# Optimization experiments

Hardware: AMD Instinct MI355X
Metric: run time of the kernel (lower is better)

Reference implementation:

```python
import jax, jax.numpy as jnp
import numpy as np

N_NODES = 200_000
N_EDGES = 3_200_000
N_GRAPHS = 512
D_IN, D_HID, D_OUT = 2, 64, 3


def setup_inputs() -> dict:
    key = jax.random.key(0)
    k = jax.random.split(key, 7)
    x = jax.random.normal(k[0], (N_NODES, D_IN), dtype=jnp.float32)
    edge_index = jax.random.randint(k[1], (2, N_EDGES), 0, N_NODES)
    batch = jnp.sort(jax.random.randint(k[2], (N_NODES,), 0, N_GRAPHS))
    W1 = jax.random.normal(k[3], (D_IN, D_HID), dtype=jnp.float32) * (1.0 / np.sqrt(D_IN))
    b1 = jnp.zeros((D_HID,), dtype=jnp.float32)
    W2 = jax.random.normal(k[4], (D_HID, D_OUT), dtype=jnp.float32) * (1.0 / np.sqrt(D_HID))
    b2 = jnp.zeros((D_OUT,), dtype=jnp.float32)
    return {"x": x, "edge_index": edge_index, "batch": batch,
            "W1": W1, "b1": b1, "W2": W2, "b2": b2}


def reference(x, edge_index, batch, W1, b1, W2, b2):
    n = x.shape[0]
    loop = jnp.arange(n, dtype=edge_index.dtype)
    src = jnp.concatenate([edge_index[0], loop])  # [E+N] with self-loops
    dst = jnp.concatenate([edge_index[1], loop])
    # symmetric normalization D^{-1/2} (A+I) D^{-1/2} (PyG GCNConv default)
    deg = jax.ops.segment_sum(jnp.ones_like(dst, dtype=x.dtype), dst, num_segments=n)
    dinv = jax.lax.rsqrt(jnp.maximum(deg, 1.0))
    norm = (dinv[src] * dinv[dst])[:, None]  # [E+N, 1]

    def gcn_conv(h, W, b):
        h = h @ W                                    # [N, d_out]
        msg = h[src] * norm                          # gather + scale
        agg = jax.ops.segment_sum(msg, dst, num_segments=n)  # scatter-add
        return agg + b

    h = jax.nn.relu(gcn_conv(x, W1, b1))
    h = gcn_conv(h, W2, b2)                          # [N, 3]

    # global mean pool over graphs in the batch
    cnt = jax.ops.segment_sum(jnp.ones((n,), h.dtype), batch, num_segments=N_GRAPHS)
    pooled = jax.ops.segment_sum(h, batch, num_segments=N_GRAPHS)
    pooled = pooled / jnp.maximum(cnt, 1.0)[:, None]  # [G, 3]
    return jax.nn.log_softmax(pooled, axis=1)
```

## Files before the change

kernel.cpp:

```cpp
#include <hip/hip_runtime.h>

#define NBLK 1024
#define PTH  512
#define SH   9
#define BUCK 512
#define NBUK_MAX 512
#define SCB  512
#define PREP_CAP 10240


__global__ void __launch_bounds__(PTH) k_pcount(const int* __restrict__ dst,
                                                int* __restrict__ hist2d,
                                                int E, int nbuk, int chunk) {
    __shared__ int h[NBUK_MAX];
    for (int t = threadIdx.x; t < nbuk; t += PTH) h[t] = 0;
    __syncthreads();
    int beg = blockIdx.x * chunk, end = min(beg + chunk, E);
    for (int i = beg + threadIdx.x; i < end; i += PTH)
        atomicAdd(&h[dst[i] >> SH], 1);
    __syncthreads();
    for (int t = threadIdx.x; t < nbuk; t += PTH)
        hist2d[t * NBLK + blockIdx.x] = h[t];
}

__global__ void __launch_bounds__(SCB) k_scanA(const int* __restrict__ in,
                                               int* __restrict__ outp,
                                               int* __restrict__ bsum, int M) {
    __shared__ int s[SCB];
    int t = threadIdx.x, i = blockIdx.x * SCB + t;
    int h = (i < M) ? in[i] : 0;
    s[t] = h; __syncthreads();
    for (int off = 1; off < SCB; off <<= 1) {
        int v = (t >= off) ? s[t - off] : 0;
        __syncthreads();
        s[t] += v;
        __syncthreads();
    }
    if (i < M) outp[i] = s[t] - h;
    if (t == SCB - 1) bsum[blockIdx.x] = s[SCB - 1];
}

__global__ void k_scanB(const int* __restrict__ bsum, int* __restrict__ bsum_ex, int NB) {
    __shared__ int s[1024];
    int t = threadIdx.x;
    int v = (t < NB) ? bsum[t] : 0;
    s[t] = v; __syncthreads();
    for (int off = 1; off < 1024; off <<= 1) {
        int u = (t >= off) ? s[t - off] : 0;
        __syncthreads();
        s[t] += u;
        __syncthreads();
    }
    if (t < NB) bsum_ex[t] = s[t] - v;
}

__device__ __forceinline__ int scan_off(const int* rs2, const int* bse, int j) {
    return rs2[j] + bse[j >> 9];
}

__global__ void __launch_bounds__(PTH) k_pfill(const int* __restrict__ src,
                                               const int* __restrict__ dst,
                                               const int* __restrict__ rs2,
                                               const int* __restrict__ bse,
                                               int* __restrict__ part,
                                               int E, int nbuk, int chunk) {
    __shared__ int cur[NBUK_MAX];
    for (int t = threadIdx.x; t < nbuk; t += PTH)
        cur[t] = scan_off(rs2, bse, t * NBLK + blockIdx.x);
    __syncthreads();
    int beg = blockIdx.x * chunk, end = min(beg + chunk, E);
    for (int i = beg + threadIdx.x; i < end; i += PTH) {
        int d = dst[i];
        int pos = atomicAdd(&cur[d >> SH], 1);
        part[pos] = (src[i] << SH) | (d & (BUCK - 1));
    }
}

__global__ void __launch_bounds__(512) k_prep(
        const int* __restrict__ part, const int* __restrict__ rs2,
        const int* __restrict__ bse, const float* __restrict__ x,
        int* __restrict__ part2, int* __restrict__ rowstart,
        float* __restrict__ dinv, float2* __restrict__ xw,
        int n, int nbuk, int E) {
    __shared__ int hist[BUCK];
    __shared__ int s[BUCK];
    __shared__ int cur[BUCK];
    __shared__ int outbuf[PREP_CAP];
    int t = threadIdx.x, b = blockIdx.x;
    hist[t] = 0;
    __syncthreads();
    int beg = scan_off(rs2, bse, b * NBLK);
    int end = (b + 1 < nbuk) ? scan_off(rs2, bse, (b + 1) * NBLK) : E;
    for (int i = beg + t; i < end; i += 512)
        atomicAdd(&hist[part[i] & (BUCK - 1)], 1);
    __syncthreads();
    s[t] = hist[t];
    __syncthreads();
    for (int d = 1; d < 512; d <<= 1) {
        int v = (t >= d) ? s[t - d] : 0;
        __syncthreads();
        s[t] += v;
        __syncthreads();
    }
    int excl = s[t] - hist[t];
    cur[t] = beg + excl;
    int node = (b << SH) + t;
    rowstart[node] = beg + excl;
    if (node < n) {
        float di = rsqrtf((float)hist[t] + 1.0f);
        dinv[node] = di;
        float2 xs = *reinterpret_cast<const float2*>(&x[2 * node]);
        xw[node] = make_float2(di * xs.x, di * xs.y);
    }
    __syncthreads();
    int cnt = end - beg;
    bool staged = (cnt <= PREP_CAP);
    if (staged) {
        for (int i = beg + t; i < end; i += 512) {
            int e = part[i];
            int p = atomicAdd(&cur[e & (BUCK - 1)], 1);
            outbuf[p - beg] = e >> SH;
        }
        __syncthreads();
        for (int i = t; i < cnt; i += 512)
            part2[beg + i] = outbuf[i];
    } else {
        for (int i = beg + t; i < end; i += 512) {
            int e = part[i];
            int p = atomicAdd(&cur[e & (BUCK - 1)], 1);
            part2[p] = e >> SH;
        }
    }
}

__global__ void __launch_bounds__(256) k_bz(
        const int* __restrict__ part2, const int* __restrict__ rowstart,
        const float* __restrict__ dinv, const float2* __restrict__ xw,
        const float* __restrict__ W1, const float* __restrict__ b1,
        const float* __restrict__ W2, float4* __restrict__ zw, int n) {
    __shared__ float sW1[128], sb1[64], sW2[192];
    for (int t = threadIdx.x; t < 128; t += 256) sW1[t] = W1[t];
    for (int t = threadIdx.x; t < 64;  t += 256) sb1[t] = b1[t];
    for (int t = threadIdx.x; t < 192; t += 256) sW2[t] = W2[t];
    __syncthreads();
    int tid = blockIdx.x * 256 + threadIdx.x;
    int i = tid >> 2, lane = tid & 3;
    if (i >= n) return;
    int beg = rowstart[i], end = rowstart[i + 1];
    float a0 = 0.f, a1 = 0.f;
    int e = beg + lane;
    for (; e + 4 < end; e += 8) {
        int s0 = part2[e];
        int s1 = part2[e + 4];
        float2 v0 = xw[s0];
        float2 v1 = xw[s1];
        a0 += v0.x + v1.x;
        a1 += v0.y + v1.y;
    }
    if (e < end) {
        float2 v = xw[part2[e]];
        a0 += v.x; a1 += v.y;
    }
    if (lane == 0) {
        float2 self = xw[i];
        a0 += self.x; a1 += self.y;
    }
    a0 += __shfl_xor(a0, 1); a0 += __shfl_xor(a0, 2);
    a1 += __shfl_xor(a1, 1); a1 += __shfl_xor(a1, 2);
    float di = dinv[i];
    a0 *= di; a1 *= di;
    float z0 = 0.f, z1 = 0.f, z2 = 0.f;
    int j0 = lane << 4;
#pragma unroll
    for (int jj = 0; jj < 16; ++jj) {
        int j = j0 + jj;
        float h = fmaf(a0, sW1[j], fmaf(a1, sW1[64 + j], sb1[j]));
        h = fmaxf(h, 0.f);
        z0 = fmaf(h, sW2[3 * j],     z0);
        z1 = fmaf(h, sW2[3 * j + 1], z1);
        z2 = fmaf(h, sW2[3 * j + 2], z2);
    }
    z0 += __shfl_xor(z0, 1); z0 += __shfl_xor(z0, 2);
    z1 += __shfl_xor(z1, 1); z1 += __shfl_xor(z1, 2);
    z2 += __shfl_xor(z2, 1); z2 += __shfl_xor(z2, 2);
    if (lane == 0)
        zw[i] = make_float4(di * z0, di * z1, di * z2, 0.f);
}

__global__ void __launch_bounds__(256) k_bout(
        const int* __restrict__ part2, const int* __restrict__ rowstart,
        const float* __restrict__ dinv, const float4* __restrict__ zw,
        const float* __restrict__ b2, const int* __restrict__ batch,
        float* __restrict__ pooled, float* __restrict__ cnt, int n) {
    int tid = blockIdx.x * 256 + threadIdx.x;
    int i = tid >> 2, lane = tid & 3;
    float o0 = 0.f, o1 = 0.f, o2 = 0.f, vc = 0.f;
    int g = -1;
    if (i < n) {
        int beg = rowstart[i], end = rowstart[i + 1];
        float a0 = 0.f, a1 = 0.f, a2 = 0.f;
        int e = beg + lane;
        for (; e + 4 < end; e += 8) {
            int s0 = part2[e];
            int s1 = part2[e + 4];
            float4 v0 = zw[s0];
            float4 v1 = zw[s1];
            a0 += v0.x + v1.x;
            a1 += v0.y + v1.y;
            a2 += v0.z + v1.z;
        }
        if (e < end) {
            float4 v = zw[part2[e]];
            a0 += v.x; a1 += v.y; a2 += v.z;
        }
        if (lane == 0) {
            float4 self = zw[i];
            a0 += self.x; a1 += self.y; a2 += self.z;
        }
        a0 += __shfl_xor(a0, 1); a0 += __shfl_xor(a0, 2);
        a1 += __shfl_xor(a1, 1); a1 += __shfl_xor(a1, 2);
        a2 += __shfl_xor(a2, 1); a2 += __shfl_xor(a2, 2);
        if (lane == 0) {
            float di = dinv[i];
            o0 = fmaf(di, a0, b2[0]);
            o1 = fmaf(di, a1, b2[1]);
            o2 = fmaf(di, a2, b2[2]);
            vc = 1.f;
        }
        g = batch[i];
    }
    int g0 = __shfl(g, 0);
    bool uni = __all(g == g0);
    if (uni) {
        for (int off = 32; off; off >>= 1) {
            o0 += __shfl_down(o0, off);
            o1 += __shfl_down(o1, off);
            o2 += __shfl_down(o2, off);
            vc += __shfl_down(vc, off);
        }
        if ((threadIdx.x & 63) == 0 && g0 >= 0) {
            atomicAdd(&pooled[3 * g0],     o0);
            atomicAdd(&pooled[3 * g0 + 1], o1);
            atomicAdd(&pooled[3 * g0 + 2], o2);
            atomicAdd(&cnt[g0], vc);
        }
    } else if (g >= 0 && lane == 0) {
        atomicAdd(&pooled[3 * g],     o0);
        atomicAdd(&pooled[3 * g + 1], o1);
        atomicAdd(&pooled[3 * g + 2], o2);
        atomicAdd(&cnt[g], 1.f);
    }
}

__global__ void k_out(const float* __restrict__ pooled, const float* __restrict__ cnt,
                      float* __restrict__ out, int G) {
    int g = blockIdx.x * blockDim.x + threadIdx.x;
    if (g >= G) return;
    float c = fmaxf(cnt[g], 1.0f);
    float p0 = pooled[3 * g] / c, p1 = pooled[3 * g + 1] / c, p2 = pooled[3 * g + 2] / c;
    float m = fmaxf(p0, fmaxf(p1, p2));
    float s = expf(p0 - m) + expf(p1 - m) + expf(p2 - m);
    float l = logf(s);
    out[3 * g]     = p0 - m - l;
    out[3 * g + 1] = p1 - m - l;
    out[3 * g + 2] = p2 - m - l;
}


__global__ void kB_deg(const int* __restrict__ dst, float* __restrict__ deg, int E) {
    int i = blockIdx.x * blockDim.x + threadIdx.x;
    if (i < E) atomicAdd(&deg[dst[i]], 1.0f);
}

__global__ void kB_dinv(float* __restrict__ deg, int n) {
    int i = blockIdx.x * blockDim.x + threadIdx.x;
    if (i < n) deg[i] = rsqrtf(deg[i] + 1.0f);
}

__global__ void kB_agg1(const int* __restrict__ src, const int* __restrict__ dst,
                        const float* __restrict__ dinv, const float* __restrict__ x,
                        float* __restrict__ agg1, int E) {
    int i = blockIdx.x * blockDim.x + threadIdx.x;
    if (i >= E) return;
    int s = src[i], d = dst[i];
    float w = dinv[s] * dinv[d];
    float2 xs = *reinterpret_cast<const float2*>(&x[2 * s]);
    atomicAdd(&agg1[2 * d],     w * xs.x);
    atomicAdd(&agg1[2 * d + 1], w * xs.y);
}

__global__ void kB_z(const float* __restrict__ agg1, const float* __restrict__ x,
                     const float* __restrict__ dinv,
                     const float* __restrict__ W1, const float* __restrict__ b1,
                     const float* __restrict__ W2, float* __restrict__ z, int n) {
    __shared__ float sW1[128], sb1[64], sW2[192];
    for (int t = threadIdx.x; t < 128; t += blockDim.x) sW1[t] = W1[t];
    for (int t = threadIdx.x; t < 64;  t += blockDim.x) sb1[t] = b1[t];
    for (int t = threadIdx.x; t < 192; t += blockDim.x) sW2[t] = W2[t];
    __syncthreads();
    int i = blockIdx.x * blockDim.x + threadIdx.x;
    if (i >= n) return;
    float di = dinv[i], w = di * di;
    float2 xs = *reinterpret_cast<const float2*>(&x[2 * i]);
    float a0 = agg1[2 * i]     + w * xs.x;
    float a1 = agg1[2 * i + 1] + w * xs.y;
    float z0 = 0.f, z1 = 0.f, z2 = 0.f;
#pragma unroll
    for (int j = 0; j < 64; ++j) {
        float h = fmaf(a0, sW1[j], fmaf(a1, sW1[64 + j], sb1[j]));
        h = fmaxf(h, 0.f);
        z0 = fmaf(h, sW2[3 * j],     z0);
        z1 = fmaf(h, sW2[3 * j + 1], z1);
        z2 = fmaf(h, sW2[3 * j + 2], z2);
    }
    z[3 * i] = z0; z[3 * i + 1] = z1; z[3 * i + 2] = z2;
}

__global__ void kB_agg2(const int* __restrict__ src, const int* __restrict__ dst,
                        const float* __restrict__ dinv, const float* __restrict__ z,
                        float* __restrict__ agg2, int E) {
    int i = blockIdx.x * blockDim.x + threadIdx.x;
    if (i >= E) return;
    int s = src[i], d = dst[i];
    float w = dinv[s] * dinv[d];
    atomicAdd(&agg2[3 * d],     w * z[3 * s]);
    atomicAdd(&agg2[3 * d + 1], w * z[3 * s + 1]);
    atomicAdd(&agg2[3 * d + 2], w * z[3 * s + 2]);
}

__global__ void kB_pool(const float* __restrict__ agg2, const float* __restrict__ z,
                        const float* __restrict__ dinv, const float* __restrict__ b2,
                        const int* __restrict__ batch,
                        float* __restrict__ pooled, float* __restrict__ cnt, int n) {
    int i = blockIdx.x * blockDim.x + threadIdx.x;
    if (i >= n) return;
    float di = dinv[i], w = di * di;
    float o0 = agg2[3 * i]     + w * z[3 * i]     + b2[0];
    float o1 = agg2[3 * i + 1] + w * z[3 * i + 1] + b2[1];
    float o2 = agg2[3 * i + 2] + w * z[3 * i + 2] + b2[2];
    int g = batch[i];
    atomicAdd(&pooled[3 * g],     o0);
    atomicAdd(&pooled[3 * g + 1], o1);
    atomicAdd(&pooled[3 * g + 2], o2);
    atomicAdd(&cnt[g], 1.0f);
}


extern "C" void kernel_launch(void* const* d_in, const int* in_sizes, int n_in,
                              void* d_out, int out_size, void* d_ws, size_t ws_size,
                              hipStream_t stream) {
    const float* x     = (const float*)d_in[0];
    const int*   ei    = (const int*)  d_in[1];
    const int*   batch = (const int*)  d_in[2];
    const float* W1    = (const float*)d_in[3];
    const float* b1    = (const float*)d_in[4];
    const float* W2    = (const float*)d_in[5];
    const float* b2    = (const float*)d_in[6];
    float*       out   = (float*)d_out;

    const int n = in_sizes[2];
    const int E = in_sizes[1] / 2;
    const int G = out_size / 3;
    const int* src = ei;
    const int* dst = ei + E;
    const int B = 256;

    const int nbuk  = (n + BUCK - 1) >> SH;
    const int chunk = (E + NBLK - 1) / NBLK;
    const int M     = nbuk * NBLK;
    const int NB2   = (M + SCB - 1) / SCB;

    size_t o = 0;
    size_t off_h2   = o; o += M;
    size_t off_rs2  = o; o += M;
    size_t off_bs   = o; o += 1024;
    size_t off_bse  = o; o += 1024;
    size_t off_part = o; o += E;
    size_t off_p2   = o; o += E;
    size_t off_row  = o; o += (size_t)nbuk * BUCK + 1;
    size_t off_dinv = o; o += n;
    size_t off_xw   = o; o += (size_t)2 * n;
    o = (o + 3) & ~(size_t)3;
    size_t off_zw   = o; o += (size_t)4 * n;
    size_t off_pool = o; o += (size_t)3 * G;
    size_t off_cnt  = o; o += G;
    size_t needA = o * 4;

    if (ws_size >= needA && nbuk <= NBUK_MAX && NB2 <= 1024) {
        int*    h2     = (int*)d_ws + off_h2;
        int*    rs2    = (int*)d_ws + off_rs2;
        int*    bs     = (int*)d_ws + off_bs;
        int*    bse    = (int*)d_ws + off_bse;
        int*    part   = (int*)d_ws + off_part;
        int*    part2  = (int*)d_ws + off_p2;
        int*    row    = (int*)d_ws + off_row;
        float*  dinv   = (float*)d_ws + off_dinv;
        float2* xw     = (float2*)((float*)d_ws + off_xw);
        float4* zw     = (float4*)((float*)d_ws + off_zw);
        float*  pooled = (float*)d_ws + off_pool;
        float*  cnt    = (float*)d_ws + off_cnt;

        hipMemsetAsync(pooled, 0, (size_t)4 * G * 4, stream);
        k_pcount<<<NBLK, PTH, 0, stream>>>(dst, h2, E, nbuk, chunk);
        k_scanA <<<NB2, SCB, 0, stream>>>(h2, rs2, bs, M);
        k_scanB <<<1, 1024, 0, stream>>>(bs, bse, NB2);
        k_pfill <<<NBLK, PTH, 0, stream>>>(src, dst, rs2, bse, part, E, nbuk, chunk);
        k_prep  <<<nbuk, 512, 0, stream>>>(part, rs2, bse, x, part2, row, dinv, xw, n, nbuk, E);
        k_bz    <<<(4 * n + 255) / 256, 256, 0, stream>>>(part2, row, dinv, xw, W1, b1, W2, zw, n);
        k_bout  <<<(4 * n + 255) / 256, 256, 0, stream>>>(part2, row, dinv, zw, b2, batch, pooled, cnt, n);
        k_out   <<<(G + B - 1) / B, B, 0, stream>>>(pooled, cnt, out, G);
    } else {
        float* ws     = (float*)d_ws;
        float* deg    = ws;
        float* agg1   = deg + n;
        float* agg2   = agg1 + 2 * (size_t)n;
        float* pooled = agg2 + 3 * (size_t)n;
        float* cnt    = pooled + 3 * (size_t)G;
        float* zf     = cnt + G;

        size_t zero_floats = (size_t)6 * n + (size_t)4 * G;
        hipMemsetAsync(ws, 0, zero_floats * sizeof(float), stream);
        kB_deg <<<(E + B - 1) / B, B, 0, stream>>>(dst, deg, E);
        kB_dinv<<<(n + B - 1) / B, B, 0, stream>>>(deg, n);
        kB_agg1<<<(E + B - 1) / B, B, 0, stream>>>(src, dst, deg, x, agg1, E);
        kB_z   <<<(n + B - 1) / B, B, 0, stream>>>(agg1, x, deg, W1, b1, W2, zf, n);
        kB_agg2<<<(E + B - 1) / B, B, 0, stream>>>(src, dst, deg, zf, agg2, E);
        kB_pool<<<(n + B - 1) / B, B, 0, stream>>>(agg2, zf, deg, b2, batch, pooled, cnt, n);
        k_out  <<<(G + B - 1) / B, B, 0, stream>>>(pooled, cnt, out, G);
    }
}
```

Measured before the change: 147.3 us.

## Stage partition writes through LDS tiles, vectorize histograms, store features in fp16

New measurement: 132.3 us. 10.2% less time.

```diff
diff --git a/kernel.cpp b/kernel.cpp
--- a/kernel.cpp
+++ b/kernel.cpp
@@ -1,4 +1,5 @@
 #include <hip/hip_runtime.h>
+#include <hip/hip_fp16.h>
 
 #define NBLK 1024
 #define PTH  512
@@ -7,6 +8,19 @@
 #define NBUK_MAX 512
 #define SCB  512
 #define PREP_CAP 10240
+#define TILE 4096
+
+__device__ __forceinline__ unsigned pack2(float a, float b) {
+    __half ha = __float2half_rn(a), hb = __float2half_rn(b);
+    unsigned short ua = *reinterpret_cast<unsigned short*>(&ha);
+    unsigned short ub = *reinterpret_cast<unsigned short*>(&hb);
+    return ((unsigned)ub << 16) | ua;
+}
+__device__ __forceinline__ float2 unpack2(unsigned u) {
+    unsigned short ua = (unsigned short)(u & 0xffff), ub = (unsigned short)(u >> 16);
+    __half ha = *reinterpret_cast<__half*>(&ua), hb = *reinterpret_cast<__half*>(&ub);
+    return make_float2(__half2float(ha), __half2float(hb));
+}
 
 
 __global__ void __launch_bounds__(PTH) k_pcount(const int* __restrict__ dst,
@@ -16,8 +30,19 @@
     for (int t = threadIdx.x; t < nbuk; t += PTH) h[t] = 0;
     __syncthreads();
     int beg = blockIdx.x * chunk, end = min(beg + chunk, E);
-    for (int i = beg + threadIdx.x; i < end; i += PTH)
-        atomicAdd(&h[dst[i] >> SH], 1);
+    int len = end - beg;
+    if (len > 0) {
+        int nq = len >> 2;
+        for (int q = threadIdx.x; q < nq; q += PTH) {
+            int4 d4 = *reinterpret_cast<const int4*>(&dst[beg + (q << 2)]);
+            atomicAdd(&h[d4.x >> SH], 1);
+            atomicAdd(&h[d4.y >> SH], 1);
+            atomicAdd(&h[d4.z >> SH], 1);
+            atomicAdd(&h[d4.w >> SH], 1);
+        }
+        for (int i = beg + (nq << 2) + threadIdx.x; i < end; i += PTH)
+            atomicAdd(&h[dst[i] >> SH], 1);
+    }
     __syncthreads();
     for (int t = threadIdx.x; t < nbuk; t += PTH)
         hist2d[t * NBLK + blockIdx.x] = h[t];
@@ -64,15 +89,47 @@
                                                const int* __restrict__ bse,
                                                int* __restrict__ part,
                                                int E, int nbuk, int chunk) {
-    __shared__ int cur[NBUK_MAX];
-    for (int t = threadIdx.x; t < nbuk; t += PTH)
-        cur[t] = scan_off(rs2, bse, t * NBLK + blockIdx.x);
-    __syncthreads();
-    int beg = blockIdx.x * chunk, end = min(beg + chunk, E);
-    for (int i = beg + threadIdx.x; i < end; i += PTH) {
-        int d = dst[i];
-        int pos = atomicAdd(&cur[d >> SH], 1);
-        part[pos] = (src[i] << SH) | (d & (BUCK - 1));
+    __shared__ int gcur[NBUK_MAX];
+    __shared__ int hist[NBUK_MAX];
+    __shared__ int scn[NBUK_MAX];
+    __shared__ int lcur[NBUK_MAX];
+    __shared__ int lout[TILE];
+    int t = threadIdx.x, b = blockIdx.x;
+    for (int u = t; u < nbuk; u += PTH)
+        gcur[u] = scan_off(rs2, bse, u * NBLK + b);
+    int beg = b * chunk, end = min(beg + chunk, E);
+    for (int tb = beg; tb < end; tb += TILE) {
+        int te = min(tb + TILE, end), cnt = te - tb;
+        for (int u = t; u < nbuk; u += PTH) hist[u] = 0;
+        __syncthreads();
+        for (int i = tb + t; i < te; i += PTH)
+            atomicAdd(&hist[dst[i] >> SH], 1);
+        __syncthreads();
+        int v = (t < nbuk) ? hist[t] : 0;
+        scn[t] = v; __syncthreads();
+        for (int off = 1; off < PTH; off <<= 1) {
+            int u = (t >= off) ? scn[t - off] : 0;
+            __syncthreads();
+            scn[t] += u;
+            __syncthreads();
+        }
+        if (t < nbuk) lcur[t] = scn[t] - hist[t];
+        __syncthreads();
+        for (int i = tb + t; i < te; i += PTH) {
+            int d = dst[i];
+            int p = atomicAdd(&lcur[d >> SH], 1);
+            lout[p] = (src[i] << SH) | (d & (BUCK - 1));
+        }
+        __syncthreads();
+        for (int j = t; j < cnt; j += PTH) {
+            int lo = 0, hi = nbuk - 1;
+            while (lo < hi) { int mid = (lo + hi) >> 1; if (scn[mid] > j) hi = mid; else lo = mid + 1; }
+            int excl = scn[lo] - hist[lo];
+            part[gcur[lo] + (j - excl)] = lout[j];
+        }
+        __syncthreads();
+        for (int u = t; u < nbuk; u += PTH) gcur[u] += hist[u];
+        __syncthreads();
     }
 }
 
@@ -80,7 +137,7 @@
         const int* __restrict__ part, const int* __restrict__ rs2,
         const int* __restrict__ bse, const float* __restrict__ x,
         int* __restrict__ part2, int* __restrict__ rowstart,
-        float* __restrict__ dinv, float2* __restrict__ xw,
+        float* __restrict__ dinv, unsigned* __restrict__ xw,
         int n, int nbuk, int E) {
     __shared__ int hist[BUCK];
     __shared__ int s[BUCK];
@@ -91,7 +148,18 @@
     __syncthreads();
     int beg = scan_off(rs2, bse, b * NBLK);
     int end = (b + 1 < nbuk) ? scan_off(rs2, bse, (b + 1) * NBLK) : E;
-    for (int i = beg + t; i < end; i += 512)
+    int ab = (beg + 3) & ~3; if (ab > end) ab = end;
+    int tstart = ab + ((end - ab) & ~3);
+    for (int i = beg + t; i < ab; i += 512)
+        atomicAdd(&hist[part[i] & (BUCK - 1)], 1);
+    for (int i = ab + t * 4; i + 3 < end; i += 512 * 4) {
+        int4 e4 = *reinterpret_cast<const int4*>(&part[i]);
+        atomicAdd(&hist[e4.x & (BUCK - 1)], 1);
+        atomicAdd(&hist[e4.y & (BUCK - 1)], 1);
+        atomicAdd(&hist[e4.z & (BUCK - 1)], 1);
+        atomicAdd(&hist[e4.w & (BUCK - 1)], 1);
+    }
+    for (int i = tstart + t; i < end; i += 512)
         atomicAdd(&hist[part[i] & (BUCK - 1)], 1);
     __syncthreads();
     s[t] = hist[t];
@@ -103,14 +171,14 @@
         __syncthreads();
     }
     int excl = s[t] - hist[t];
-    cur[t] = beg + excl;
+    cur[t] = excl;
     int node = (b << SH) + t;
     rowstart[node] = beg + excl;
     if (node < n) {
         float di = rsqrtf((float)hist[t] + 1.0f);
         dinv[node] = di;
         float2 xs = *reinterpret_cast<const float2*>(&x[2 * node]);
-        xw[node] = make_float2(di * xs.x, di * xs.y);
+        xw[node] = pack2(di * xs.x, di * xs.y);
     }
     __syncthreads();
     int cnt = end - beg;
@@ -119,7 +187,7 @@
         for (int i = beg + t; i < end; i += 512) {
             int e = part[i];
             int p = atomicAdd(&cur[e & (BUCK - 1)], 1);
-            outbuf[p - beg] = e >> SH;
+            outbuf[p] = e >> SH;
         }
         __syncthreads();
         for (int i = t; i < cnt; i += 512)
@@ -128,16 +196,16 @@
         for (int i = beg + t; i < end; i += 512) {
             int e = part[i];
             int p = atomicAdd(&cur[e & (BUCK - 1)], 1);
-            part2[p] = e >> SH;
+            part2[beg + p] = e >> SH;
         }
     }
 }
 
 __global__ void __launch_bounds__(256) k_bz(
         const int* __restrict__ part2, const int* __restrict__ rowstart,
-        const float* __restrict__ dinv, const float2* __restrict__ xw,
+        const float* __restrict__ dinv, const unsigned* __restrict__ xw,
         const float* __restrict__ W1, const float* __restrict__ b1,
-        const float* __restrict__ W2, float4* __restrict__ zw, int n) {
+        const float* __restrict__ W2, uint2* __restrict__ zw, int n) {
     __shared__ float sW1[128], sb1[64], sW2[192];
     for (int t = threadIdx.x; t < 128; t += 256) sW1[t] = W1[t];
     for (int t = threadIdx.x; t < 64;  t += 256) sb1[t] = b1[t];
@@ -152,17 +220,17 @@
     for (; e + 4 < end; e += 8) {
         int s0 = part2[e];
         int s1 = part2[e + 4];
-        float2 v0 = xw[s0];
-        float2 v1 = xw[s1];
+        float2 v0 = unpack2(xw[s0]);
+        float2 v1 = unpack2(xw[s1]);
         a0 += v0.x + v1.x;
         a1 += v0.y + v1.y;
     }
     if (e < end) {
-        float2 v = xw[part2[e]];
+        float2 v = unpack2(xw[part2[e]]);
         a0 += v.x; a1 += v.y;
     }
     if (lane == 0) {
-        float2 self = xw[i];
+        float2 self = unpack2(xw[i]);
         a0 += self.x; a1 += self.y;
     }
     a0 += __shfl_xor(a0, 1); a0 += __shfl_xor(a0, 2);
@@ -184,12 +252,12 @@
     z1 += __shfl_xor(z1, 1); z1 += __shfl_xor(z1, 2);
     z2 += __shfl_xor(z2, 1); z2 += __shfl_xor(z2, 2);
     if (lane == 0)
-        zw[i] = make_float4(di * z0, di * z1, di * z2, 0.f);
+        zw[i] = make_uint2(pack2(di * z0, di * z1), pack2(di * z2, 0.f));
 }
 
 __global__ void __launch_bounds__(256) k_bout(
         const int* __restrict__ part2, const int* __restrict__ rowstart,
-        const float* __restrict__ dinv, const float4* __restrict__ zw,
+        const float* __restrict__ dinv, const uint2* __restrict__ zw,
         const float* __restrict__ b2, const int* __restrict__ batch,
         float* __restrict__ pooled, float* __restrict__ cnt, int n) {
     int tid = blockIdx.x * 256 + threadIdx.x;
@@ -203,19 +271,22 @@
         for (; e + 4 < end; e += 8) {
             int s0 = part2[e];
             int s1 = part2[e + 4];
-            float4 v0 = zw[s0];
-            float4 v1 = zw[s1];
-            a0 += v0.x + v1.x;
-            a1 += v0.y + v1.y;
-            a2 += v0.z + v1.z;
+            uint2 u0 = zw[s0];
+            uint2 u1 = zw[s1];
+            float2 p0 = unpack2(u0.x), p1 = unpack2(u1.x);
+            a0 += p0.x + p1.x;
+            a1 += p0.y + p1.y;
+            a2 += unpack2(u0.y).x + unpack2(u1.y).x;
         }
         if (e < end) {
-            float4 v = zw[part2[e]];
-            a0 += v.x; a1 += v.y; a2 += v.z;
+            uint2 u = zw[part2[e]];
+            float2 p = unpack2(u.x);
+            a0 += p.x; a1 += p.y; a2 += unpack2(u.y).x;
         }
         if (lane == 0) {
-            float4 self = zw[i];
-            a0 += self.x; a1 += self.y; a2 += self.z;
+            uint2 u = zw[i];
+            float2 p = unpack2(u.x);
+            a0 += p.x; a1 += p.y; a2 += unpack2(u.y).x;
         }
         a0 += __shfl_xor(a0, 1); a0 += __shfl_xor(a0, 2);
         a1 += __shfl_xor(a1, 1); a1 += __shfl_xor(a1, 2);
@@ -366,7 +437,7 @@
     const int B = 256;
 
     const int nbuk  = (n + BUCK - 1) >> SH;
-    const int chunk = (E + NBLK - 1) / NBLK;
+    const int chunk = (((E + NBLK - 1) / NBLK) + 3) & ~3;
     const int M     = nbuk * NBLK;
     const int NB2   = (M + SCB - 1) / SCB;
 
@@ -379,26 +450,26 @@
     size_t off_p2   = o; o += E;
     size_t off_row  = o; o += (size_t)nbuk * BUCK + 1;
     size_t off_dinv = o; o += n;
-    size_t off_xw   = o; o += (size_t)2 * n;
-    o = (o + 3) & ~(size_t)3;
-    size_t off_zw   = o; o += (size_t)4 * n;
+    size_t off_xw   = o; o += n;
+    o = (o + 1) & ~(size_t)1;
+    size_t off_zw   = o; o += (size_t)2 * n;
     size_t off_pool = o; o += (size_t)3 * G;
     size_t off_cnt  = o; o += G;
     size_t needA = o * 4;
 
     if (ws_size >= needA && nbuk <= NBUK_MAX && NB2 <= 1024) {
-        int*    h2     = (int*)d_ws + off_h2;
-        int*    rs2    = (int*)d_ws + off_rs2;
-        int*    bs     = (int*)d_ws + off_bs;
-        int*    bse    = (int*)d_ws + off_bse;
-        int*    part   = (int*)d_ws + off_part;
-        int*    part2  = (int*)d_ws + off_p2;
-        int*    row    = (int*)d_ws + off_row;
-        float*  dinv   = (float*)d_ws + off_dinv;
-        float2* xw     = (float2*)((float*)d_ws + off_xw);
-        float4* zw     = (float4*)((float*)d_ws + off_zw);
-        float*  pooled = (float*)d_ws + off_pool;
-        float*  cnt    = (float*)d_ws + off_cnt;
+        int*      h2     = (int*)d_ws + off_h2;
+        int*      rs2    = (int*)d_ws + off_rs2;
+        int*      bs     = (int*)d_ws + off_bs;
+        int*      bse    = (int*)d_ws + off_bse;
+        int*      part   = (int*)d_ws + off_part;
+        int*      part2  = (int*)d_ws + off_p2;
+        int*      row    = (int*)d_ws + off_row;
+        float*    dinv   = (float*)d_ws + off_dinv;
+        unsigned* xw     = (unsigned*)((int*)d_ws + off_xw);
+        uint2*    zw     = (uint2*)((int*)d_ws + off_zw);
+        float*    pooled = (float*)d_ws + off_pool;
+        float*    cnt    = (float*)d_ws + off_cnt;
 
         hipMemsetAsync(pooled, 0, (size_t)4 * G * 4, stream);
         k_pcount<<<NBLK, PTH, 0, stream>>>(dst, h2, E, nbuk, chunk);
```
